# Kernel tuning notes

Hardware: AMD Instinct MI355X
Metric: run time of the kernel (lower is better)

The kernel has to match this reference:

```python
import jax, jax.numpy as jnp
import numpy as np

NEG_INF = float('-inf')
B, T, C, U = 32, 1000, 500, 100
RISK_FACTOR = 0.1  # risk_strategy='exp', group_strategy='end'


def _lse3(x1, x2, x3):
    # numerically-safe logsumexp of 3 args, nan-free grads at -inf
    m = jnp.maximum(jnp.maximum(x1, x2), x3)
    dead = jnp.isneginf(m)
    ms = jnp.where(dead, 0.0, m)
    s = jnp.exp(x1 - ms) + jnp.exp(x2 - ms) + jnp.exp(x3 - ms)
    s = jnp.where(dead, 1.0, s)
    return jnp.where(dead, NEG_INF, ms + jnp.log(s))


def _safe_lse(x, axis):
    m = jnp.max(x, axis=axis, keepdims=True)
    dead = jnp.isneginf(m)
    ms = jnp.where(dead, 0.0, m)
    s = jnp.sum(jnp.exp(x - ms), axis=axis, keepdims=True)
    s = jnp.where(dead, 1.0, s)
    out = jnp.where(dead, NEG_INF, ms + jnp.log(s))
    return jnp.squeeze(out, axis)


def _log_sub_exp(a, b):
    # faithful port of espnet's log_substraction_exp: log(exp(a)-exp(b))
    mask1 = (~jnp.isinf(a)) & (~jnp.isinf(b))
    a_ = jnp.where(mask1, a, -1.0)
    b_ = jnp.where(mask1, b, -2.0)
    ans_tmp = b_ + jnp.log(jnp.exp(a_ - b_) - 1.0)
    a2 = jnp.where(jnp.isinf(ans_tmp), -2000.0, a_)
    b2 = jnp.where(jnp.isinf(ans_tmp), -2001.0, b_)
    ans1 = b2 + jnp.log(jnp.exp(a2 - b2) - 1.0)
    ans = jnp.where(mask1, ans1, jnp.full_like(a, NEG_INF))
    mask2 = (~jnp.isinf(a)) & jnp.isinf(b)
    return jnp.where(mask2, a, ans)


def _shift_r(x, n):
    return jnp.pad(x[:, :-n], ((0, 0), (n, 0)), constant_values=NEG_INF)


def _shift_l(x, n):
    return jnp.pad(x[:, n:], ((0, 0), (0, n)), constant_values=NEG_INF)


def _brctc_loss(nnet_output, ys_pad, hlens, ylens):
    # Dense equivalent of the k2 CTC lattice forward-backward in the log semiring.
    Bb, Tt, Cc = nnet_output.shape
    Uu = ys_pad.shape[1]
    S = 2 * Uu + 1  # extended label states: blank,y1,blank,...,yU,blank
    dt = nnet_output.dtype
    s_idx = jnp.arange(S)
    lab = ys_pad[:, jnp.clip((s_idx - 1) // 2, 0, Uu - 1)]        # [B,S]
    labels_ext = jnp.where((s_idx % 2 == 1)[None, :], lab, 0)
    prev_lab = ys_pad[:, jnp.clip((s_idx - 3) // 2, 0, Uu - 1)]
    allow_skip = ((s_idx % 2 == 1) & (s_idx >= 3))[None, :] & (lab != prev_lab)
    # p_ext[b,t,s] = nnet_output[b,t,labels_ext[b,s]]
    p_ext = jnp.take_along_axis(
        nnet_output, jnp.broadcast_to(labels_ext[:, None, :], (Bb, Tt, S)), axis=2)
    valid_s = s_idx[None, :] <= 2 * ylens[:, None]                # states beyond 2*ylen don't exist
    p_ext = jnp.where(valid_s[:, None, :], p_ext, NEG_INF)
    p_tbs = jnp.transpose(p_ext, (1, 0, 2))                       # [T,B,S]

    # forward: alpha[t,s] includes emission at frame t
    def fstep(a, pt):
        anew = pt + _lse3(a, _shift_r(a, 1),
                          jnp.where(allow_skip, _shift_r(a, 2), NEG_INF))
        return anew, anew
    a0 = jnp.full((Bb, S), NEG_INF, dt).at[:, 0].set(0.0)  # virtual start state
    _, alpha = jax.lax.scan(fstep, a0, p_tbs)                     # [T,B,S]

    # backward: beta[t,s] covers frames t+1..hlen-1 (excludes emission at t)
    t_arr = jnp.arange(Tt)
    fin = (s_idx[None, :] == 2 * ylens[:, None]) | (s_idx[None, :] == 2 * ylens[:, None] - 1)
    beta_fin = jnp.where(fin, 0.0, NEG_INF).astype(dt)
    allow_skip_n2 = jnp.pad(allow_skip[:, 2:], ((0, 0), (0, 2)), constant_values=False)
    p_next = jnp.concatenate([p_tbs[1:], jnp.full((1, Bb, S), NEG_INF, dt)], axis=0)

    def bstep(bcarry, inp):
        t, pn = inp
        q = pn + bcarry
        cand = _lse3(q, _shift_l(q, 1),
                     jnp.where(allow_skip_n2, _shift_l(q, 2), NEG_INF))
        bnew = jnp.where((t == hlens - 1)[:, None], beta_fin, cand)
        return bnew, bnew
    _, beta = jax.lax.scan(bstep, jnp.full((Bb, S), NEG_INF, dt),
                           (t_arr, p_next), reverse=True)         # [T,B,S]

    alpha = jnp.transpose(alpha, (1, 2, 0))                       # [B,S,T]
    beta = jnp.transpose(beta, (1, 2, 0))
    alpha = jnp.where((t_arr[None, :] < hlens[:, None])[:, None, :], alpha, NEG_INF)

    # keep only label (odd) states, as in alpha[:, 1::2]
    a_l = alpha[:, 1::2, :]
    b_l = beta[:, 1::2, :]
    p_l = jnp.transpose(p_ext, (0, 2, 1))[:, 1::2, :]
    dead = jnp.isneginf(a_l)  # states absent from the lattice
    b_l = jnp.where(dead, NEG_INF, b_l)
    p_l = jnp.where(dead, NEG_INF, p_l)

    # beta' removes the self-loop continuation -> posterior of label u ending at t
    beta_prime = _log_sub_exp(b_l[:, :, :-1], b_l[:, :, 1:] + p_l[:, :, 1:])
    beta_prime = jnp.concatenate([beta_prime, b_l[:, :, -1:]], axis=-1)
    loss_state = a_l + beta_prime                                 # [B,U,T]

    # risk_strategy == 'exp': risk = -risk_factor * t / hlen
    risk = -RISK_FACTOR * (t_arr[None, None, :].astype(dt) / hlens[:, None, None].astype(dt))
    loss_state = loss_state + risk

    loss_u = _safe_lse(loss_state, 2)                             # [B,U]
    mask = ~jnp.isneginf(loss_u)
    last = jnp.sum(mask.astype(jnp.int32), axis=1) - 1            # = ylen-1
    loss = jnp.take_along_axis(loss_u, last[:, None], axis=1)[:, 0]
    return -loss


def setup_inputs():
    key = jax.random.key(0)
    k1, k2, k3, k4 = jax.random.split(key, 4)
    nnet_output = jax.nn.log_softmax(
        jax.random.normal(k1, (B, T, C), dtype=jnp.float32), axis=-1)
    ys_pad = jax.random.randint(k2, (B, U), 1, C, dtype=jnp.int32)  # labels, 0 = blank excluded
    ylens = jax.random.randint(k3, (B,), 80, U + 1, dtype=jnp.int32)
    hlens = jax.random.randint(k4, (B,), 800, T + 1, dtype=jnp.int32)
    return {'nnet_output': nnet_output, 'ys_pad': ys_pad, 'hlens': hlens, 'ylens': ylens}


def reference(nnet_output, ys_pad, hlens, ylens):
    return _brctc_loss(nnet_output, ys_pad, hlens, ylens)
```

## Files before the change

### kernel.cpp

```cpp
#include <hip/hip_runtime.h>
#include <math.h>

#define T_DIM 1000
#define C_DIM 500
#define U_DIM 100
#define PAD   16
#define AROWS (T_DIM + 5)
#define NEGINF (-INFINITY)
#define LROW  120

typedef float v2f __attribute__((ext_vector_type(2)));
__device__ __forceinline__ v2f mk2(float x, float y) { v2f r; r[0] = x; r[1] = y; return r; }
#define PKMAX(a, b) __builtin_elementwise_max((a), (b))

__device__ __forceinline__ v2f dual_lse(float aE, float bE,
                                        float x1, float x2, float x3) {
    v2f t1 = PKMAX(mk2(aE, x1), mk2(bE, x2));
    float mO = fmaxf(t1[1], x3);
    float mnE = fminf(aE, bE);
    v2f m = mk2(t1[0], mO);
    v2f d1 = mk2(mnE, x1) - m;
    v2f d2 = mk2(x2, x3) - mk2(mO, mO);
    float eE = __expf(d1[0]);
    float e1 = __expf(d1[1]);
    float e2 = __expf(d2[0]);
    float e3 = __expf(d2[1]);
    v2f s = mk2(1.0f, e1) + mk2(eE, e2);
    float sO = s[1] + e3;
    float lE = __logf(s[0]);
    float lO = __logf(sO);
    v2f r = m + mk2(lE, lO);
    return PKMAX(r, mk2(NEGINF, NEGINF));
}

__device__ __forceinline__ float lse3f(float x1, float x2, float x3) {
    float m = fmaxf(fmaxf(x1, x2), x3);
    if (m == NEGINF) return NEGINF;
    return m + __logf(__expf(x1 - m) + __expf(x2 - m) + __expf(x3 - m));
}

__device__ __forceinline__ float log_sub_expf(float a, float b) {
    bool ia = isinf(a), ib = isinf(b);
    if (!ia && !ib) {
        float ans = b + __logf(__expf(a - b) - 1.0f);
        if (isinf(ans)) ans = -2001.0f + __logf(__expf(1.0f) - 1.0f);
        return ans;
    }
    if (!ia && ib) return a;
    return NEGINF;
}

__device__ __forceinline__ float dpp_shr1(float x) {
    int r = __builtin_amdgcn_update_dpp(__float_as_int(NEGINF), __float_as_int(x),
                                        0x138, 0xF, 0xF, false);
    return __int_as_float(r);
}
__device__ __forceinline__ float dpp_shl1(float x) {
    int r = __builtin_amdgcn_update_dpp(__float_as_int(NEGINF), __float_as_int(x),
                                        0x130, 0xF, 0xF, false);
    return __int_as_float(r);
}

#define LSTEP(tt, RA, RB, RP)                                                \
    {                                                                        \
        float a_nx = (RA), br_nx = (RB), p_nx = (RP);                        \
        float bl   = (a_t  == NEGINF) ? NEGINF : braw_t;                     \
        float term = (a_nx == NEGINF) ? NEGINF : (br_nx + p_nx);             \
        float bp = log_sub_expf(bl, term);                                   \
        float x = a_t + bp - 0.1f * (float)(tt) * inv_hl;                    \
        if (x != NEGINF) {                                                   \
            float nm = fmaxf(m, x);                                          \
            ssum = ssum * __expf(m - nm) + __expf(x - nm);                   \
            m = nm;                                                          \
        }                                                                    \
        a_t = a_nx; braw_t = br_nx;                                          \
    }

__device__ __forceinline__ void gather_chunk(
    const float* __restrict__ nb, const int* __restrict__ shY, int yl,
    float* __restrict__ lds, float* __restrict__ ldsb,
    float* __restrict__ Pg ,
    int row0, int j)
{
#pragma unroll
    for (int k = 0; k < 17; ++k) {
        int i = j + k * 384;
        if (i < 6400) {
            int r = i >> 7, q = i & 127;
            if (q <= 100) {
                int row = row0 + r;
                int col = (q < 100) ? shY[q] : 0;
                float v = (row < T_DIM) ? nb[(size_t)row * C_DIM + col] : NEGINF;
                if (q < 100) {
                    lds[r * LROW + q] = (q < yl) ? v : NEGINF;
                    if (Pg) Pg[(size_t)r * U_DIM + q] = v;
                } else {
                    ldsb[r] = v;
                }
            }
        }
    }
}


#define FWP(j, pOv, gv)                                                      \
    {                                                                        \
        float Osh = dpp_shr1(O0);                                            \
        v2f r = dual_lse(E0, Osh, O0, E0, Osh + mskFlo);                     \
        v2f N = mk2(mzE_lo + (gv), (pOv)) + r;                               \
        float nOsh = dpp_shr1(N[1]);                                         \
        if (L == 50)                                                         \
            ((float2*)rlyF)[(tbk + (j)) & 127] = make_float2(nOsh, N[0]);    \
        E0 = N[0]; O0 = N[1];                                                \
        if (st) stA[(j) * U_DIM] = N[1];                                     \
    }

#define FWC(j, pOv, gv, rv)                                                  \
    {                                                                        \
        float Esh = dpp_shr1(E0); Esh = (L == 0) ? (rv).y : Esh;             \
        float Osh = dpp_shr1(O0); Osh = (L == 0) ? (rv).x : Osh;             \
        v2f r = dual_lse(E0, O0, O0, Esh, Osh + mskFhi);                     \
        v2f N = mk2(mzE_hi + (gv), (pOv)) + r;                               \
        E0 = N[0]; O0 = N[1];                                                \
        if (st) stA[(j) * U_DIM] = N[1];                                     \
    }

#define BWP(j, pOv, gv, FINF)                                                \
    {                                                                        \
        const int t_ = tbk - (j);                                            \
        v2f q = mk2(mzE_hi + (gv), (pOv)) + mk2(BE, BO);                     \
        if (L == 0) rlyB[(999 - t_) & 127] = q[1];                           \
        float qOsh = dpp_shl1(q[1]);                                         \
        v2f r = dual_lse(q[0], qOsh, q[1], q[0], qOsh + mskBhi);             \
        if (FINF) { const bool fin = (t_ == hl1);                            \
            BE = fin ? fE_hi : r[0]; BO = fin ? fO_hi : r[1];                \
        } else { BE = r[0]; BO = r[1]; }                                     \
        if (st) stB[-(int)((j) * U_DIM)] = BO;                               \
    }

#define BWC(j, pOv, gv, FINF, rq)                                            \
    {                                                                        \
        const int t_ = tbk - (j);                                            \
        v2f q = mk2(mzE_lo + (gv), (pOv)) + mk2(BE, BO);                     \
        float qO = (L == 50) ? (rq) : q[1];                                  \
        float qEsh = dpp_shl1(q[0]);                                         \
        float qOsh = dpp_shl1(qO);                                           \
        v2f r = dual_lse(q[0], qO, qO, qEsh, qOsh + mskBlo);                 \
        if (FINF) { const bool fin = (t_ == hl1);                            \
            BE = fin ? fE_lo : r[0]; BO = fin ? fO_lo : r[1];                \
        } else { BE = r[0]; BO = r[1]; }                                     \
        if (st) stB[-(int)((j) * U_DIM)] = BO;                               \
    }

#define BWP_BLOCK(FINF)                                                      \
    {                                                                        \
        const int tbk = tb2 + kk;                                            \
        float p0 = bb2[(kk-0)*LROW + 50 + L], p1 = bb2[(kk-1)*LROW + 50 + L],\
              p2 = bb2[(kk-2)*LROW + 50 + L], p3 = bb2[(kk-3)*LROW + 50 + L],\
              p4 = bb2[(kk-4)*LROW + 50 + L], p5 = bb2[(kk-5)*LROW + 50 + L],\
              p6 = bb2[(kk-6)*LROW + 50 + L], p7 = bb2[(kk-7)*LROW + 50 + L],\
              p8 = bb2[(kk-8)*LROW + 50 + L], p9 = bb2[(kk-9)*LROW + 50 + L];\
        float g0 = bp2[kk-0], g1 = bp2[kk-1], g2 = bp2[kk-2], g3 = bp2[kk-3],\
              g4 = bp2[kk-4], g5 = bp2[kk-5], g6 = bp2[kk-6], g7 = bp2[kk-7],\
              g8 = bp2[kk-8], g9 = bp2[kk-9];                                \
        BWP(0,p0,g0,FINF) BWP(1,p1,g1,FINF) BWP(2,p2,g2,FINF)                \
        BWP(3,p3,g3,FINF) BWP(4,p4,g4,FINF) BWP(5,p5,g5,FINF)                \
        BWP(6,p6,g6,FINF) BWP(7,p7,g7,FINF) BWP(8,p8,g8,FINF)                \
        BWP(9,p9,g9,FINF)                                                    \
        stB -= 10 * U_DIM;                                                   \
    }

#define BWC_BLOCK(FINF)                                                      \
    {                                                                        \
        const int tbk = tb2 + kk;                                            \
        const int kb = 999 - tbk;                                            \
        float q0 = rlyB[(kb+0)&127], q1 = rlyB[(kb+1)&127],                  \
              q2 = rlyB[(kb+2)&127], q3 = rlyB[(kb+3)&127],                  \
              q4 = rlyB[(kb+4)&127], q5 = rlyB[(kb+5)&127],                  \
              q6 = rlyB[(kb+6)&127], q7 = rlyB[(kb+7)&127],                  \
              q8 = rlyB[(kb+8)&127], q9 = rlyB[(kb+9)&127];                  \
        float p0 = bb2[(kk-0)*LROW + L], p1 = bb2[(kk-1)*LROW + L],          \
              p2 = bb2[(kk-2)*LROW + L], p3 = bb2[(kk-3)*LROW + L],          \
              p4 = bb2[(kk-4)*LROW + L], p5 = bb2[(kk-5)*LROW + L],          \
              p6 = bb2[(kk-6)*LROW + L], p7 = bb2[(kk-7)*LROW + L],          \
              p8 = bb2[(kk-8)*LROW + L], p9 = bb2[(kk-9)*LROW + L];          \
        float g0 = bp2[kk-0], g1 = bp2[kk-1], g2 = bp2[kk-2], g3 = bp2[kk-3],\
              g4 = bp2[kk-4], g5 = bp2[kk-5], g6 = bp2[kk-6], g7 = bp2[kk-7],\
              g8 = bp2[kk-8], g9 = bp2[kk-9];                                \
        BWC(0,p0,g0,FINF,q0) BWC(1,p1,g1,FINF,q1) BWC(2,p2,g2,FINF,q2)       \
        BWC(3,p3,g3,FINF,q3) BWC(4,p4,g4,FINF,q4) BWC(5,p5,g5,FINF,q5)       \
        BWC(6,p6,g6,FINF,q6) BWC(7,p7,g7,FINF,q7) BWC(8,p8,g8,FINF,q8)       \
        BWC(9,p9,g9,FINF,q9)                                                 \
        stB -= 10 * U_DIM;                                                   \
    }

extern "C" __global__ void __launch_bounds__(1024)
brctc_fused(const float* __restrict__ nnet, const int* __restrict__ ys,
            const int* __restrict__ hlens, const int* __restrict__ ylens,
            float* __restrict__ P,
            float* __restrict__ A, float* __restrict__ Braw,
            float* __restrict__ out)
{
    const int b = blockIdx.x;
    const int tid = threadIdx.x;
    const int w = tid >> 6, L = tid & 63;
    const int hl = hlens[b], yl = ylens[b];
    const int hl1 = hl - 1;
    const size_t TP = T_DIM + 2 * PAD;
    const float* nb = nnet + (size_t)b * T_DIM * C_DIM;
    float* Pw = P + ((size_t)b * TP + PAD) * U_DIM;
    const float* Pb = Pw;
    const int* ysb = ys + b * U_DIM;
    float* Ab = A    + (size_t)b * AROWS * U_DIM;
    float* Bb = Braw + (size_t)b * AROWS * U_DIM;

    __shared__ __align__(16) float fbuf[3][50 * LROW];
    __shared__ __align__(16) float bbuf[3][50 * LROW];
    __shared__ float fpb[3][56], bpb[3][56];
    __shared__ float shm[8][U_DIM], shs[8][U_DIM], shlu[U_DIM];
    __shared__ int shY[U_DIM];
    __shared__ __align__(8) float rlyF[256];
    __shared__ float rlyB[128];

    if (tid < U_DIM) shY[tid] = ysb[tid];

    const int cl = U_DIM - 1;
    const int yL   = ysb[min(L, cl)];
    const int yLm1 = ysb[min(max(L - 1, 0), cl)];
    const int yLp1 = ysb[min(L + 1, cl)];
    const int y50L = ysb[min(50 + L, cl)];
    const int y49L = ysb[min(49 + L, cl)];
    const int y51L = ysb[min(51 + L, cl)];
    const int ty = 2 * yl;
    const bool st = (L < 50);
    const float mzE_lo = (L <= 50 && 2 * L <= ty)       ? 0.0f : NEGINF;
    const float mzE_hi = (L <= 49 && 102 + 2 * L <= ty) ? 0.0f : NEGINF;
    const float mskFlo = (L >= 1 && yL != yLm1)  ? 0.0f : NEGINF;
    const float mskFhi = (y50L != y49L)          ? 0.0f : NEGINF;
    const float mskBhi = (L <= 48 && y51L != y50L) ? 0.0f : NEGINF;
    const float mskBlo = (yLp1 != yL)            ? 0.0f : NEGINF;
    const float fE_lo = (2*L     == ty || 2*L     == ty-1) ? 0.0f : NEGINF;
    const float fO_lo = (2*L+1   == ty || 2*L+1   == ty-1) ? 0.0f : NEGINF;
    const float fE_hi = (102+2*L == ty || 102+2*L == ty-1) ? 0.0f : NEGINF;
    const float fO_hi = (101+2*L == ty || 101+2*L == ty-1) ? 0.0f : NEGINF;

    float E0, O0, BE, BO;
    E0 = (w == 0 && L == 0) ? 0.0f : NEGINF;
    O0 = NEGINF; BE = NEGINF; BO = NEGINF;

    __syncthreads();

    if (w == 0 && L == 0)
        ((float2*)rlyF)[127] = make_float2(NEGINF, NEGINF);
    if (w >= 4) {
        int j2 = tid - 256;
        for (int i = j2; i < 6 * 50 * 20; i += 768) {
            int buf = i / 1000, rem = i % 1000;
            int r = rem / 20, q = 100 + rem % 20;
            float* base = (buf == 0) ? fbuf[0] : (buf == 1) ? fbuf[1]
                        : (buf == 2) ? fbuf[2] : (buf == 3) ? bbuf[0]
                        : (buf == 4) ? bbuf[1] : bbuf[2];
            base[r * LROW + q] = NEGINF;
        }
    }
    if (w >= 4 && w < 10) {
        int j = tid - 256;
        gather_chunk(nb, shY, yl, fbuf[0], fpb[0], Pw, 0, j);
        if (j < U_DIM) Pw[(size_t)T_DIM * U_DIM + j] = NEGINF;
    } else if (w >= 10) {
        int j = tid - 640;
        gather_chunk(nb, shY, yl, bbuf[0], bpb[0], nullptr, 951, j);
    }
    __syncthreads();

    for (int i = 0; i < 21; ++i) {
        if (w == 0) {
            if (i < 20) {
                const float* fb = fbuf[i % 3];
                const float* fp = fpb[i % 3];
                const int tb = 50 * i;
                float* stA = Ab + (size_t)tb * U_DIM + L;
                for (int kk = 0; kk < 50; kk += 10) {
                    const int tbk = tb + kk;
                    float p0 = fb[(kk+0)*LROW + L], p1 = fb[(kk+1)*LROW + L],
                          p2 = fb[(kk+2)*LROW + L], p3 = fb[(kk+3)*LROW + L],
                          p4 = fb[(kk+4)*LROW + L], p5 = fb[(kk+5)*LROW + L],
                          p6 = fb[(kk+6)*LROW + L], p7 = fb[(kk+7)*LROW + L],
                          p8 = fb[(kk+8)*LROW + L], p9 = fb[(kk+9)*LROW + L];
                    float g0 = fp[kk+0], g1 = fp[kk+1], g2 = fp[kk+2],
                          g3 = fp[kk+3], g4 = fp[kk+4], g5 = fp[kk+5],
                          g6 = fp[kk+6], g7 = fp[kk+7], g8 = fp[kk+8],
                          g9 = fp[kk+9];
                    FWP(0,p0,g0) FWP(1,p1,g1) FWP(2,p2,g2) FWP(3,p3,g3)
                    FWP(4,p4,g4) FWP(5,p5,g5) FWP(6,p6,g6) FWP(7,p7,g7)
                    FWP(8,p8,g8) FWP(9,p9,g9)
                    stA += 10 * U_DIM;
                }
            }
        } else if (w == 1) {
            if (i >= 1) {
                const int ci = i - 1;
                const float* fb = fbuf[ci % 3];
                const float* fp = fpb[ci % 3];
                const int tb = 50 * ci;
                float* stA = Ab + (size_t)tb * U_DIM + 50 + L;
                for (int kk = 0; kk < 50; kk += 10) {
                    const int tbk = tb + kk;
                    const float2* rf = (const float2*)rlyF;
                    float2 v0 = rf[(tbk + 127) & 127], v1 = rf[(tbk + 0) & 127],
                           v2 = rf[(tbk + 1) & 127],   v3 = rf[(tbk + 2) & 127],
                           v4 = rf[(tbk + 3) & 127],   v5 = rf[(tbk + 4) & 127],
                           v6 = rf[(tbk + 5) & 127],   v7 = rf[(tbk + 6) & 127],
                           v8 = rf[(tbk + 7) & 127],   v9 = rf[(tbk + 8) & 127];
                    float p0 = fb[(kk+0)*LROW + 50 + L], p1 = fb[(kk+1)*LROW + 50 + L],
                          p2 = fb[(kk+2)*LROW + 50 + L], p3 = fb[(kk+3)*LROW + 50 + L],
                          p4 = fb[(kk+4)*LROW + 50 + L], p5 = fb[(kk+5)*LROW + 50 + L],
                          p6 = fb[(kk+6)*LROW + 50 + L], p7 = fb[(kk+7)*LROW + 50 + L],
                          p8 = fb[(kk+8)*LROW + 50 + L], p9 = fb[(kk+9)*LROW + 50 + L];
                    float g0 = fp[kk+0], g1 = fp[kk+1], g2 = fp[kk+2],
                          g3 = fp[kk+3], g4 = fp[kk+4], g5 = fp[kk+5],
                          g6 = fp[kk+6], g7 = fp[kk+7], g8 = fp[kk+8],
                          g9 = fp[kk+9];
                    FWC(0,p0,g0,v0) FWC(1,p1,g1,v1) FWC(2,p2,g2,v2) FWC(3,p3,g3,v3)
                    FWC(4,p4,g4,v4) FWC(5,p5,g5,v5) FWC(6,p6,g6,v6) FWC(7,p7,g7,v7)
                    FWC(8,p8,g8,v8) FWC(9,p9,g9,v9)
                    stA += 10 * U_DIM;
                }
            }
        } else if (w == 2) {
            if (i < 20) {
                const float* bb2 = bbuf[i % 3];
                const float* bp2 = bpb[i % 3];
                const int cc = 19 - i;
                const int tb2 = 50 * cc;
                float* stB = Bb + (size_t)(tb2 + 49) * U_DIM + 50 + L;
                if (hl1 >= tb2 && hl1 <= tb2 + 49) {
                    for (int kk = 49; kk >= 9; kk -= 10) BWP_BLOCK(true)
                } else {
                    for (int kk = 49; kk >= 9; kk -= 10) BWP_BLOCK(false)
                }
            }
        } else if (w == 3) {
            if (i >= 1) {
                const int ci = i - 1;
                const float* bb2 = bbuf[ci % 3];
                const float* bp2 = bpb[ci % 3];
                const int cc = 19 - ci;
                const int tb2 = 50 * cc;
                float* stB = Bb + (size_t)(tb2 + 49) * U_DIM + L;
                if (hl1 >= tb2 && hl1 <= tb2 + 49) {
                    for (int kk = 49; kk >= 9; kk -= 10) BWC_BLOCK(true)
                } else {
                    for (int kk = 49; kk >= 9; kk -= 10) BWC_BLOCK(false)
                }
            }
        } else if (i < 19) {
            const int bi = (i + 1) % 3;
            if (w < 10) {
                int j = tid - 256;
                int row0 = (i + 1) * 50;
                gather_chunk(nb, shY, yl, fbuf[bi], fpb[bi],
                             Pw + (size_t)row0 * U_DIM, row0, j);
            } else {
                int j = tid - 640;
                int row0 = (18 - i) * 50 + 1;
                gather_chunk(nb, shY, yl, bbuf[bi], bpb[bi],
                             nullptr, row0, j);
            }
        }
        __syncthreads();
    }

    if (w == 0 && st)
        ((float2*)(Ab + (size_t)T_DIM * U_DIM))[L] = make_float2(NEGINF, NEGINF);

    {
        const int r0f = min(hl, T_DIM);
        const int nrow = T_DIM + 1 - r0f;
        const int tot = nrow * 50;
        for (int i = tid; i < tot; i += 1024) {
            const int rr = r0f + i / 50, cc2 = i % 50;
            ((float2*)(Ab + (size_t)rr * U_DIM))[cc2] = make_float2(NEGINF, NEGINF);
        }
    }
    __syncthreads();

    {
        const int u = tid & 127;
        const int c = tid >> 7;
        if (u < U_DIM) {
            const bool valu = (u < yl);
            const float inv_hl = 1.0f / (float)hl;
            const int t0 = 125 * c;
            float a_t    = Ab[(size_t)t0 * U_DIM + u];
            float braw_t = Bb[(size_t)t0 * U_DIM + u];
            float aA0 = Ab[(long)(t0 + 1) * U_DIM + u];
            float aA1 = Ab[(long)(t0 + 2) * U_DIM + u];
            float aA2 = Ab[(long)(t0 + 3) * U_DIM + u];
            float aA3 = Ab[(long)(t0 + 4) * U_DIM + u];
            float bA0 = Bb[(long)(t0 + 1) * U_DIM + u];
            float bA1 = Bb[(long)(t0 + 2) * U_DIM + u];
            float bA2 = Bb[(long)(t0 + 3) * U_DIM + u];
            float bA3 = Bb[(long)(t0 + 4) * U_DIM + u];
            float pA0 = valu ? Pb[(long)(t0 + 1) * U_DIM + u] : NEGINF;
            float pA1 = valu ? Pb[(long)(t0 + 2) * U_DIM + u] : NEGINF;
            float pA2 = valu ? Pb[(long)(t0 + 3) * U_DIM + u] : NEGINF;
            float pA3 = valu ? Pb[(long)(t0 + 4) * U_DIM + u] : NEGINF;
            float m = NEGINF, ssum = 0.0f;
            for (int kb = 0; kb <= 120; kb += 4) {
                long nr = (long)(t0 + kb + 5);
                float aB0 = Ab[(nr + 0) * U_DIM + u];
                float aB1 = Ab[(nr + 1) * U_DIM + u];
                float aB2 = Ab[(nr + 2) * U_DIM + u];
                float aB3 = Ab[(nr + 3) * U_DIM + u];
                float bB0 = Bb[(nr + 0) * U_DIM + u];
                float bB1 = Bb[(nr + 1) * U_DIM + u];
                float bB2 = Bb[(nr + 2) * U_DIM + u];
                float bB3 = Bb[(nr + 3) * U_DIM + u];
                float pB0 = valu ? Pb[(nr + 0) * U_DIM + u] : NEGINF;
                float pB1 = valu ? Pb[(nr + 1) * U_DIM + u] : NEGINF;
                float pB2 = valu ? Pb[(nr + 2) * U_DIM + u] : NEGINF;
                float pB3 = valu ? Pb[(nr + 3) * U_DIM + u] : NEGINF;
                LSTEP(t0 + kb + 0, aA0, bA0, pA0)
                LSTEP(t0 + kb + 1, aA1, bA1, pA1)
                LSTEP(t0 + kb + 2, aA2, bA2, pA2)
                LSTEP(t0 + kb + 3, aA3, bA3, pA3)
                aA0 = aB0; aA1 = aB1; aA2 = aB2; aA3 = aB3;
                bA0 = bB0; bA1 = bB1; bA2 = bB2; bA3 = bB3;
                pA0 = pB0; pA1 = pB1; pA2 = pB2; pA3 = pB3;
            }
            LSTEP(t0 + 124, aA0, bA0, pA0)
            shm[c][u] = m; shs[c][u] = ssum;
        }
    }
    __syncthreads();
    if (tid < U_DIM) {
        float M = NEGINF;
#pragma unroll
        for (int c = 0; c < 8; ++c) M = fmaxf(M, shm[c][tid]);
        float lu = NEGINF;
        if (M != NEGINF) {
            float s = 0.0f;
#pragma unroll
            for (int c = 0; c < 8; ++c) {
                float mc = shm[c][tid];
                if (mc != NEGINF) s += shs[c][tid] * __expf(mc - M);
            }
            lu = M + __logf(s);
        }
        shlu[tid] = lu;
    }
    __syncthreads();
    if (tid == 0) {
        int cnt = 0;
        for (int u = 0; u < U_DIM; ++u) cnt += (shlu[u] != NEGINF) ? 1 : 0;
        int last = cnt - 1;
        last = last < 0 ? 0 : (last > U_DIM - 1 ? U_DIM - 1 : last);
        out[b] = -shlu[last];
    }
}

extern "C" __global__ void __launch_bounds__(256)
brctc_fwd_fb(const float* __restrict__ nnet, const int* __restrict__ ys,
             const int* __restrict__ hlens, const int* __restrict__ ylens,
             float* __restrict__ a_l)
{
    const int b = blockIdx.x;
    const int s = threadIdx.x;
    __shared__ float sh_a[201];
    __shared__ int   sh_ys[U_DIM];
    if (s < U_DIM) sh_ys[s] = ys[b * U_DIM + s];
    __syncthreads();
    const int hl = hlens[b], yl = ylens[b];
    int lab = 0; bool skip = false;
    if (s < 201) {
        if (s & 1) lab = sh_ys[(s - 1) >> 1];
        if ((s & 1) && s >= 3) skip = (sh_ys[(s - 1) >> 1] != sh_ys[(s - 3) >> 1]);
        sh_a[s] = (s == 0) ? 0.0f : NEGINF;
    }
    const bool valid = (s < 201) && (s <= 2 * yl);
    const bool isodd = (s < 201) && (s & 1);
    const int l = (s - 1) >> 1;
    const float* base = nnet + (size_t)b * T_DIM * C_DIM;
    float* alb = a_l + (size_t)b * T_DIM * U_DIM;
    __syncthreads();
    float p_cur = valid ? base[lab] : NEGINF;
    for (int t = 0; t < T_DIM; ++t) {
        float p_nxt = (valid && (t + 1 < T_DIM)) ? base[(size_t)(t + 1) * C_DIM + lab] : NEGINF;
        float x1 = (s < 201) ? sh_a[s] : NEGINF;
        float x2 = (s >= 1 && s < 201) ? sh_a[s - 1] : NEGINF;
        float x3 = skip ? sh_a[s - 2] : NEGINF;
        float anew = p_cur + lse3f(x1, x2, x3);
        __syncthreads();
        if (s < 201) sh_a[s] = anew;
        if (isodd) alb[t * U_DIM + l] = (t < hl) ? anew : NEGINF;
        __syncthreads();
        p_cur = p_nxt;
    }
}

extern "C" __global__ void __launch_bounds__(256)
brctc_bwd_fb(const float* __restrict__ nnet, const int* __restrict__ ys,
             const int* __restrict__ hlens, const int* __restrict__ ylens,
             const float* __restrict__ a_l, float* __restrict__ out)
{
    const int b = blockIdx.x;
    const int s = threadIdx.x;
    __shared__ float sh_b[201], sh_q[201], sh_lu[U_DIM];
    __shared__ int sh_ys[U_DIM];
    if (s < U_DIM) sh_ys[s] = ys[b * U_DIM + s];
    __syncthreads();
    const int hl = hlens[b], yl = ylens[b];
    int lab = 0; bool skip2 = false;
    if (s < 201) {
        if (s & 1) lab = sh_ys[(s - 1) >> 1];
        int s2 = s + 2;
        if (s2 < 201 && (s2 & 1) && s2 >= 3)
            skip2 = (sh_ys[(s2 - 1) >> 1] != sh_ys[(s2 - 3) >> 1]);
        sh_b[s] = NEGINF;
    }
    const bool valid = (s < 201) && (s <= 2 * yl);
    const bool isodd = (s < 201) && (s & 1);
    const int l = (s - 1) >> 1;
    const float fin0 = (s == 2 * yl || s == 2 * yl - 1) ? 0.0f : NEGINF;
    const float* base = nnet + (size_t)b * T_DIM * C_DIM;
    const float* alb = a_l + (size_t)b * T_DIM * U_DIM;
    float m_run = NEGINF, acc = 0.0f, prev_bl = NEGINF, p_hi = NEGINF;
    __syncthreads();
    for (int t = T_DIM - 1; t >= 0; --t) {
        float p_lo = valid ? base[(size_t)t * C_DIM + lab] : NEGINF;
        float a_cur = isodd ? alb[t * U_DIM + l] : NEGINF;
        float q = (s < 201) ? (p_hi + sh_b[s]) : NEGINF;
        if (s < 201) sh_q[s] = q;
        __syncthreads();
        float q2 = (s + 1 < 201) ? sh_q[s + 1] : NEGINF;
        float q3 = skip2 ? sh_q[s + 2] : NEGINF;
        float cand = lse3f(q, q2, q3);
        float bnew = (t == hl - 1) ? fin0 : cand;
        if (s < 201) sh_b[s] = bnew;
        if (isodd) {
            float bl_t = (a_cur == NEGINF) ? NEGINF : bnew;
            float bp = (t == T_DIM - 1) ? bl_t : log_sub_expf(bl_t, prev_bl + p_hi);
            float x = a_cur + bp - 0.1f * ((float)t / (float)hl);
            if (x != NEGINF) {
                if (x <= m_run) acc += __expf(x - m_run);
                else { acc = acc * __expf(m_run - x) + 1.0f; m_run = x; }
            }
            prev_bl = bl_t;
        }
        __syncthreads();
        p_hi = p_lo;
    }
    if (isodd) sh_lu[l] = (m_run == NEGINF) ? NEGINF : (m_run + __logf(acc));
    __syncthreads();
    if (s == 0) {
        int cnt = 0;
        for (int u = 0; u < U_DIM; ++u) cnt += (sh_lu[u] != NEGINF) ? 1 : 0;
        int last = cnt - 1;
        last = last < 0 ? 0 : (last > U_DIM - 1 ? U_DIM - 1 : last);
        out[b] = -sh_lu[last];
    }
}

extern "C" void kernel_launch(void* const* d_in, const int* in_sizes, int n_in,
                              void* d_out, int out_size, void* d_ws, size_t ws_size,
                              hipStream_t stream) {
    const float* nnet  = (const float*)d_in[0];
    const int*   ys    = (const int*)d_in[1];
    const int*   hlens = (const int*)d_in[2];
    const int*   ylens = (const int*)d_in[3];
    float*       outp  = (float*)d_out;
    const int B = in_sizes[2];
    const size_t TP = T_DIM + 2 * PAD;
    const size_t szP  = (size_t)B * TP * U_DIM;
    const size_t szA  = (size_t)B * AROWS * U_DIM;
    const size_t need = (szP + 2 * szA) * sizeof(float);

    if (ws_size >= need) {
        float* P    = (float*)d_ws;
        float* A    = P + szP;
        float* Braw = A + szA;
        brctc_fused<<<B, 1024, 0, stream>>>(nnet, ys, hlens, ylens, P, A, Braw, outp);
    } else {
        float* A = (float*)d_ws;
        brctc_fwd_fb<<<B, 256, 0, stream>>>(nnet, ys, hlens, ylens, A);
        brctc_bwd_fb<<<B, 256, 0, stream>>>(nnet, ys, hlens, ylens, A, outp);
    }
}
```

Before: 349.8 us.

## Overlap loss-segment accumulation with forward/backward recursion using idle gather waves

Moves the per-segment loss logsumexp accumulation into the main time loop so waves that only gather can advance segments whose alpha/beta rows are already final. Each of segments 1-6 gets a fixed start iteration, processes 8 four-row blocks per iteration, and keeps its state in registers; segments 0 and 7 and any leftover work finish after the loop. The goal is to shrink the serial loss tail after the recursion. In exchange it adds register pressure, a hardcoded schedule that depends on hl for segment 6, and removes the explicit NEGINF write of the row at T.

```diff
diff --git a/kernel.cpp b/kernel.cpp
--- a/kernel.cpp
+++ b/kernel.cpp
@@ -75,6 +75,61 @@
         }                                                                    \
         a_t = a_nx; braw_t = br_nx;                                          \
     }
+
+__device__ __forceinline__ void loss_chain(
+    const float* __restrict__ Ab, const float* __restrict__ Bb,
+    const float* __restrict__ Pb, int t0, int u, bool valu, float inv_hl,
+    int& kb, float& m, float& ssum, float& a_t, float& braw_t,
+    float& aA0, float& aA1, float& aA2, float& aA3,
+    float& bA0, float& bA1, float& bA2, float& bA3,
+    float& pA0, float& pA1, float& pA2, float& pA3,
+    int nblk, float* __restrict__ smp, float* __restrict__ ssp)
+{
+    if (kb < 0) {
+        a_t    = Ab[(long)t0 * U_DIM + u];
+        braw_t = Bb[(long)t0 * U_DIM + u];
+        aA0 = Ab[(long)(t0 + 1) * U_DIM + u];
+        aA1 = Ab[(long)(t0 + 2) * U_DIM + u];
+        aA2 = Ab[(long)(t0 + 3) * U_DIM + u];
+        aA3 = Ab[(long)(t0 + 4) * U_DIM + u];
+        bA0 = Bb[(long)(t0 + 1) * U_DIM + u];
+        bA1 = Bb[(long)(t0 + 2) * U_DIM + u];
+        bA2 = Bb[(long)(t0 + 3) * U_DIM + u];
+        bA3 = Bb[(long)(t0 + 4) * U_DIM + u];
+        pA0 = valu ? Pb[(long)(t0 + 1) * U_DIM + u] : NEGINF;
+        pA1 = valu ? Pb[(long)(t0 + 2) * U_DIM + u] : NEGINF;
+        pA2 = valu ? Pb[(long)(t0 + 3) * U_DIM + u] : NEGINF;
+        pA3 = valu ? Pb[(long)(t0 + 4) * U_DIM + u] : NEGINF;
+        m = NEGINF; ssum = 0.0f;
+        kb = 0;
+    }
+    while (nblk > 0 && kb <= 124) {
+        if (kb <= 120) {
+            long nr = (long)(t0 + kb + 5);
+            float aB0 = Ab[(nr + 0) * U_DIM + u], aB1 = Ab[(nr + 1) * U_DIM + u],
+                  aB2 = Ab[(nr + 2) * U_DIM + u], aB3 = Ab[(nr + 3) * U_DIM + u];
+            float bB0 = Bb[(nr + 0) * U_DIM + u], bB1 = Bb[(nr + 1) * U_DIM + u],
+                  bB2 = Bb[(nr + 2) * U_DIM + u], bB3 = Bb[(nr + 3) * U_DIM + u];
+            float pB0 = valu ? Pb[(nr + 0) * U_DIM + u] : NEGINF;
+            float pB1 = valu ? Pb[(nr + 1) * U_DIM + u] : NEGINF;
+            float pB2 = valu ? Pb[(nr + 2) * U_DIM + u] : NEGINF;
+            float pB3 = valu ? Pb[(nr + 3) * U_DIM + u] : NEGINF;
+            LSTEP(t0 + kb + 0, aA0, bA0, pA0)
+            LSTEP(t0 + kb + 1, aA1, bA1, pA1)
+            LSTEP(t0 + kb + 2, aA2, bA2, pA2)
+            LSTEP(t0 + kb + 3, aA3, bA3, pA3)
+            aA0 = aB0; aA1 = aB1; aA2 = aB2; aA3 = aB3;
+            bA0 = bB0; bA1 = bB1; bA2 = bB2; bA3 = bB3;
+            pA0 = pB0; pA1 = pB1; pA2 = pB2; pA3 = pB3;
+            kb += 4;
+        } else {
+            LSTEP(t0 + 124, aA0, bA0, pA0)
+            *smp = m; *ssp = ssum;
+            kb = 128;
+        }
+        --nblk;
+    }
+}
 
 __device__ __forceinline__ void gather_chunk(
     const float* __restrict__ nb, const int* __restrict__ shY, int yl,
@@ -102,7 +157,6 @@
     }
 }
 
-
 #define FWP(j, pOv, gv)                                                      \
     {                                                                        \
         float Osh = dpp_shr1(O0);                                            \
@@ -173,12 +227,12 @@
 #define BWC_BLOCK(FINF)                                                      \
     {                                                                        \
         const int tbk = tb2 + kk;                                            \
-        const int kb = 999 - tbk;                                            \
-        float q0 = rlyB[(kb+0)&127], q1 = rlyB[(kb+1)&127],                  \
-              q2 = rlyB[(kb+2)&127], q3 = rlyB[(kb+3)&127],                  \
-              q4 = rlyB[(kb+4)&127], q5 = rlyB[(kb+5)&127],                  \
-              q6 = rlyB[(kb+6)&127], q7 = rlyB[(kb+7)&127],                  \
-              q8 = rlyB[(kb+8)&127], q9 = rlyB[(kb+9)&127];                  \
+        const int kb_ = 999 - tbk;                                           \
+        float q0 = rlyB[(kb_+0)&127], q1 = rlyB[(kb_+1)&127],                \
+              q2 = rlyB[(kb_+2)&127], q3 = rlyB[(kb_+3)&127],                \
+              q4 = rlyB[(kb_+4)&127], q5 = rlyB[(kb_+5)&127],                \
+              q6 = rlyB[(kb_+6)&127], q7 = rlyB[(kb_+7)&127],                \
+              q8 = rlyB[(kb_+8)&127], q9 = rlyB[(kb_+9)&127];                \
         float p0 = bb2[(kk-0)*LROW + L], p1 = bb2[(kk-1)*LROW + L],          \
               p2 = bb2[(kk-2)*LROW + L], p3 = bb2[(kk-3)*LROW + L],          \
               p4 = bb2[(kk-4)*LROW + L], p5 = bb2[(kk-5)*LROW + L],          \
@@ -206,6 +260,7 @@
     const int w = tid >> 6, L = tid & 63;
     const int hl = hlens[b], yl = ylens[b];
     const int hl1 = hl - 1;
+    const float inv_hl = 1.0f / (float)hl;
     const size_t TP = T_DIM + 2 * PAD;
     const float* nb = nnet + (size_t)b * T_DIM * C_DIM;
     float* Pw = P + ((size_t)b * TP + PAD) * U_DIM;
@@ -247,6 +302,26 @@
     float E0, O0, BE, BO;
     E0 = (w == 0 && L == 0) ? 0.0f : NEGINF;
     O0 = NEGINF; BE = NEGINF; BO = NEGINF;
+
+    const int lg  = (tid - 256) >> 7;
+    const int ug  = (tid - 256) & 127;
+    int myseg = 0, mystart = 0;
+    switch (lg) {
+        case 0: myseg = 3; mystart = 14; break;
+        case 1: myseg = 4; mystart = 14; break;
+        case 2: myseg = 2; mystart = 16; break;
+        case 3: myseg = 5; mystart = 17; break;
+        case 4: myseg = 1; mystart = 19; break;
+        default: myseg = 6; mystart = 19; break;
+    }
+    const bool lossOK  = (tid >= 256) && (ug < U_DIM);
+    const bool mayHide = (myseg != 6) || (hl > 879);
+    const bool valu_g  = (ug < yl);
+    int   lkb = -1;
+    float lm = 0, lss = 0, lat = 0, lbt = 0;
+    float lA0 = 0, lA1 = 0, lA2 = 0, lA3 = 0;
+    float lB0 = 0, lB1 = 0, lB2 = 0, lB3 = 0;
+    float lP0 = 0, lP1 = 0, lP2 = 0, lP3 = 0;
 
     __syncthreads();
 
@@ -354,25 +429,30 @@
                     for (int kk = 49; kk >= 9; kk -= 10) BWC_BLOCK(false)
                 }
             }
-        } else if (i < 19) {
-            const int bi = (i + 1) % 3;
-            if (w < 10) {
-                int j = tid - 256;
-                int row0 = (i + 1) * 50;
-                gather_chunk(nb, shY, yl, fbuf[bi], fpb[bi],
-                             Pw + (size_t)row0 * U_DIM, row0, j);
-            } else {
-                int j = tid - 640;
-                int row0 = (18 - i) * 50 + 1;
-                gather_chunk(nb, shY, yl, bbuf[bi], bpb[bi],
-                             nullptr, row0, j);
-            }
+        } else {
+            if (i < 19) {
+                const int bi = (i + 1) % 3;
+                if (w < 10) {
+                    int j = tid - 256;
+                    int row0 = (i + 1) * 50;
+                    gather_chunk(nb, shY, yl, fbuf[bi], fpb[bi],
+                                 Pw + (size_t)row0 * U_DIM, row0, j);
+                } else {
+                    int j = tid - 640;
+                    int row0 = (18 - i) * 50 + 1;
+                    gather_chunk(nb, shY, yl, bbuf[bi], bpb[bi],
+                                 nullptr, row0, j);
+                }
+            }
+            if (lossOK && mayHide && i >= mystart)
+                loss_chain(Ab, Bb, Pb, 125 * myseg, ug, valu_g, inv_hl,
+                           lkb, lm, lss, lat, lbt,
+                           lA0, lA1, lA2, lA3, lB0, lB1, lB2, lB3,
+                           lP0, lP1, lP2, lP3,
+                           8, &shm[myseg][ug], &shs[myseg][ug]);
         }
         __syncthreads();
     }
-
-    if (w == 0 && st)
-        ((float2*)(Ab + (size_t)T_DIM * U_DIM))[L] = make_float2(NEGINF, NEGINF);
 
     {
         const int r0f = min(hl, T_DIM);
@@ -385,52 +465,26 @@
     }
     __syncthreads();
 
-    {
-        const int u = tid & 127;
-        const int c = tid >> 7;
-        if (u < U_DIM) {
-            const bool valu = (u < yl);
-            const float inv_hl = 1.0f / (float)hl;
-            const int t0 = 125 * c;
-            float a_t    = Ab[(size_t)t0 * U_DIM + u];
-            float braw_t = Bb[(size_t)t0 * U_DIM + u];
-            float aA0 = Ab[(long)(t0 + 1) * U_DIM + u];
-            float aA1 = Ab[(long)(t0 + 2) * U_DIM + u];
-            float aA2 = Ab[(long)(t0 + 3) * U_DIM + u];
-            float aA3 = Ab[(long)(t0 + 4) * U_DIM + u];
-            float bA0 = Bb[(long)(t0 + 1) * U_DIM + u];
-            float bA1 = Bb[(long)(t0 + 2) * U_DIM + u];
-            float bA2 = Bb[(long)(t0 + 3) * U_DIM + u];
-            float bA3 = Bb[(long)(t0 + 4) * U_DIM + u];
-            float pA0 = valu ? Pb[(long)(t0 + 1) * U_DIM + u] : NEGINF;
-            float pA1 = valu ? Pb[(long)(t0 + 2) * U_DIM + u] : NEGINF;
-            float pA2 = valu ? Pb[(long)(t0 + 3) * U_DIM + u] : NEGINF;
-            float pA3 = valu ? Pb[(long)(t0 + 4) * U_DIM + u] : NEGINF;
-            float m = NEGINF, ssum = 0.0f;
-            for (int kb = 0; kb <= 120; kb += 4) {
-                long nr = (long)(t0 + kb + 5);
-                float aB0 = Ab[(nr + 0) * U_DIM + u];
-                float aB1 = Ab[(nr + 1) * U_DIM + u];
-                float aB2 = Ab[(nr + 2) * U_DIM + u];
-                float aB3 = Ab[(nr + 3) * U_DIM + u];
-                float bB0 = Bb[(nr + 0) * U_DIM + u];
-                float bB1 = Bb[(nr + 1) * U_DIM + u];
-                float bB2 = Bb[(nr + 2) * U_DIM + u];
-                float bB3 = Bb[(nr + 3) * U_DIM + u];
-                float pB0 = valu ? Pb[(nr + 0) * U_DIM + u] : NEGINF;
-                float pB1 = valu ? Pb[(nr + 1) * U_DIM + u] : NEGINF;
-                float pB2 = valu ? Pb[(nr + 2) * U_DIM + u] : NEGINF;
-                float pB3 = valu ? Pb[(nr + 3) * U_DIM + u] : NEGINF;
-                LSTEP(t0 + kb + 0, aA0, bA0, pA0)
-                LSTEP(t0 + kb + 1, aA1, bA1, pA1)
-                LSTEP(t0 + kb + 2, aA2, bA2, pA2)
-                LSTEP(t0 + kb + 3, aA3, bA3, pA3)
-                aA0 = aB0; aA1 = aB1; aA2 = aB2; aA3 = aB3;
-                bA0 = bB0; bA1 = bB1; bA2 = bB2; bA3 = bB3;
-                pA0 = pB0; pA1 = pB1; pA2 = pB2; pA3 = pB3;
-            }
-            LSTEP(t0 + 124, aA0, bA0, pA0)
-            shm[c][u] = m; shs[c][u] = ssum;
+    if (tid >= 256) {
+        if (lossOK)
+            loss_chain(Ab, Bb, Pb, 125 * myseg, ug, valu_g, inv_hl,
+                       lkb, lm, lss, lat, lbt,
+                       lA0, lA1, lA2, lA3, lB0, lB1, lB2, lB3,
+                       lP0, lP1, lP2, lP3,
+                       64, &shm[myseg][ug], &shs[myseg][ug]);
+    } else {
+        const int cseg = (tid >> 7) ? 7 : 0;
+        const int u2 = tid & 127;
+        if (u2 < U_DIM) {
+            int   kb2 = -1;
+            float m2 = 0, ss2 = 0, at2 = 0, bt2 = 0;
+            float a0 = 0, a1 = 0, a2 = 0, a3 = 0;
+            float b0 = 0, b1 = 0, b2 = 0, b3 = 0;
+            float q0 = 0, q1 = 0, q2 = 0, q3 = 0;
+            loss_chain(Ab, Bb, Pb, 125 * cseg, u2, (u2 < yl), inv_hl,
+                       kb2, m2, ss2, at2, bt2,
+                       a0, a1, a2, a3, b0, b1, b2, b3, q0, q1, q2, q3,
+                       64, &shm[cseg][u2], &shs[cseg][u2]);
         }
     }
     __syncthreads();
```

Result: slower. 456.2 us (+30.4%).
